# Kernel tuning notes

Hardware: AMD Instinct MI355X
Metric: run time of the kernel (lower is better)

The kernel has to match this reference:

```python
import jax, jax.numpy as jnp
import numpy as np

N_LEVELS = 16
N_FEATS = 2
LOG2_HASHMAP_SIZE = 19
BASE_RES = np.float32(16.0)
FINEST_RES = np.float32(512.0)
N_POINTS = 1048576

# corner offsets in (i, j, k) order: index = i*4 + j*2 + k, matching BOX_OFFSETS
OFFSETS = jnp.array([[i, j, k] for i in (0, 1) for j in (0, 1) for k in (0, 1)], dtype=jnp.int32)  # [8,3]
# spatial-hash primes from HashNeRF / Instant-NGP
PRIMES = np.array([1, 2654435761, 805459861], dtype=np.uint32)
HASH_MASK = np.uint32((1 << LOG2_HASHMAP_SIZE) - 1)


def _hash(coords):
    # coords: [..., 3] int32 grid coords -> [...] int32 table index
    c = coords.astype(jnp.uint32)
    h = (c[..., 0] * PRIMES[0]) ^ (c[..., 1] * PRIMES[1]) ^ (c[..., 2] * PRIMES[2])
    return (h & HASH_MASK).astype(jnp.int32)


def setup_inputs() -> dict:
    key = jax.random.key(0)
    k1, k2, k3 = jax.random.split(key, 3)
    x = jax.random.uniform(k1, (N_POINTS, 3), dtype=jnp.float32)  # points in unit box
    # nn.init.uniform_(weight, -1e-4, 1e-4), stacked over levels
    embeddings = jax.random.uniform(
        k2, (N_LEVELS, 1 << LOG2_HASHMAP_SIZE, N_FEATS),
        dtype=jnp.float32, minval=-1e-4, maxval=1e-4)
    level_weights = jnp.zeros((N_LEVELS,), dtype=jnp.float32)
    box_min = jnp.zeros((3,), dtype=jnp.float32)
    box_max = jnp.ones((3,), dtype=jnp.float32)
    return {"x": x, "embeddings": embeddings, "level_weights": level_weights,
            "box_min": box_min, "box_max": box_max}


def reference(x, embeddings, level_weights, box_min, box_max):
    n_levels = embeddings.shape[0]
    # per-level growth factor b = exp((log(finest) - log(base)) / (L-1)), static
    b = np.float32(np.exp((np.log(FINEST_RES) - np.log(BASE_RES)) / (n_levels - 1)))
    xc = jnp.clip(x, box_min, box_max)  # [N,3]
    outs = []
    for i in range(n_levels):
        res = np.float32(np.floor(BASE_RES * b ** i))  # static scalar resolution
        grid = (box_max - box_min) / res               # [3]
        bl = jnp.floor((xc - box_min) / grid).astype(jnp.int32)  # [N,3] bottom-left cell
        vmin = bl.astype(jnp.float32) * grid + box_min           # [N,3]
        vmax = vmin + grid                                       # [N,3]
        idx = _hash(bl[:, None, :] + OFFSETS[None, :, :])        # [N,8]
        emb = embeddings[i][idx]                                 # [N,8,F] gather
        # trilinear interpolation (weights use raw x, as in the torch module)
        w = (x - vmin) / (vmax - vmin)                           # [N,3]
        wx = w[:, 0][:, None, None]                              # [N,1,1]
        wy = w[:, 1][:, None]
        wz = w[:, 2][:, None]
        cx = emb[:, 0:4] * (1 - wx) + emb[:, 4:8] * wx           # [N,4,F] blend x
        c0 = cx[:, 0] * (1 - wy) + cx[:, 2] * wy                 # [N,F] blend y (k=0)
        c1 = cx[:, 1] * (1 - wy) + cx[:, 3] * wy                 # [N,F] blend y (k=1)
        c = c0 * (1 - wz) + c1 * wz                              # [N,F] blend z
        gate = jax.nn.sigmoid(level_weights[i])
        outs.append(c * gate)
    return jnp.concatenate(outs, axis=-1)  # [N, L*F]
```

## Files before the change

### kernel.cpp

```cpp
#include <hip/hip_runtime.h>
#include <stdint.h>


static constexpr int NP = 1048576;
static constexpr int NL = 16;
static constexpr int TPB = 256;
static constexpr uint32_t HMASK = (1u << 19) - 1u;

__constant__ float c_res[NL] = {16.f, 20.f, 25.f, 32.f, 40.f, 50.f, 64.f, 80.f,
                                101.f, 128.f, 161.f, 203.f, 256.f, 322.f, 406.f, 512.f};

__device__ __forceinline__ float2 enc_one(
    float x0, float x1, float x2,
    float b0, float b1, float b2,
    float B0, float B1, float B2,
    const float2* __restrict__ tab, float res, float gate)
{
    float g0 = (B0 - b0) / res;
    float g1 = (B1 - b1) / res;
    float g2 = (B2 - b2) / res;
    float xc0 = fminf(fmaxf(x0, b0), B0);
    float xc1 = fminf(fmaxf(x1, b1), B1);
    float xc2 = fminf(fmaxf(x2, b2), B2);
    float f0 = floorf((xc0 - b0) / g0);
    float f1 = floorf((xc1 - b1) / g1);
    float f2 = floorf((xc2 - b2) / g2);
    float v0 = f0 * g0 + b0;
    float v1 = f1 * g1 + b1;
    float v2 = f2 * g2 + b2;
    float w0 = (x0 - v0) / ((v0 + g0) - v0);
    float w1 = (x1 - v1) / ((v1 + g1) - v1);
    float w2 = (x2 - v2) / ((v2 + g2) - v2);

    uint32_t u0 = (uint32_t)(int)f0;
    uint32_t u1 = (uint32_t)(int)f1;
    uint32_t u2 = (uint32_t)(int)f2;
    uint32_t ya = u1 * 2654435761u, yb = (u1 + 1u) * 2654435761u;
    uint32_t za = u2 * 805459861u,  zb = (u2 + 1u) * 805459861u;
    uint32_t xa = u0, xb = u0 + 1u;

    float2 e000 = tab[(xa ^ ya ^ za) & HMASK];
    float2 e001 = tab[(xa ^ ya ^ zb) & HMASK];
    float2 e010 = tab[(xa ^ yb ^ za) & HMASK];
    float2 e011 = tab[(xa ^ yb ^ zb) & HMASK];
    float2 e100 = tab[(xb ^ ya ^ za) & HMASK];
    float2 e101 = tab[(xb ^ ya ^ zb) & HMASK];
    float2 e110 = tab[(xb ^ yb ^ za) & HMASK];
    float2 e111 = tab[(xb ^ yb ^ zb) & HMASK];

    float s0 = 1.f - w0, s1 = 1.f - w1, s2 = 1.f - w2;
    float cx00x = e000.x * s0 + e100.x * w0, cx00y = e000.y * s0 + e100.y * w0;
    float cx01x = e001.x * s0 + e101.x * w0, cx01y = e001.y * s0 + e101.y * w0;
    float cx10x = e010.x * s0 + e110.x * w0, cx10y = e010.y * s0 + e110.y * w0;
    float cx11x = e011.x * s0 + e111.x * w0, cx11y = e011.y * s0 + e111.y * w0;
    float c0x = cx00x * s1 + cx10x * w1, c0y = cx00y * s1 + cx10y * w1;
    float c1x = cx01x * s1 + cx11x * w1, c1y = cx01y * s1 + cx11y * w1;
    float ox = c0x * s2 + c1x * w2;
    float oy = c0y * s2 + c1y * w2;
    return make_float2(ox * gate, oy * gate);
}

__global__ __launch_bounds__(TPB) void k_enc(
    const float* __restrict__ x, const float* __restrict__ emb,
    const float* __restrict__ lw, const float* __restrict__ bmin,
    const float* __restrict__ bmax, float2* __restrict__ ws)
{
    int p = blockIdx.x * TPB + threadIdx.x;
    int l = blockIdx.y;
    float x0 = x[3 * p + 0], x1 = x[3 * p + 1], x2 = x[3 * p + 2];
    float b0 = bmin[0], b1 = bmin[1], b2 = bmin[2];
    float B0 = bmax[0], B1 = bmax[1], B2 = bmax[2];
    float res = c_res[l];
    float gate = 1.0f / (1.0f + expf(-lw[l]));
    const float2* tab = (const float2*)(emb + ((size_t)l << 20));
    float2 r = enc_one(x0, x1, x2, b0, b1, b2, B0, B1, B2, tab, res, gate);
    ws[(size_t)l * NP + p] = r;
}

__global__ __launch_bounds__(TPB) void k_tr(
    const float2* __restrict__ ws, float4* __restrict__ out)
{
    __shared__ float2 s[256][17];
    int t = threadIdx.x;
    size_t p0 = (size_t)blockIdx.x * 256;
#pragma unroll
    for (int l = 0; l < NL; ++l)
        s[t][l] = ws[(size_t)l * NP + p0 + (size_t)t];
    __syncthreads();
#pragma unroll
    for (int k = 0; k < 8; ++k) {
        int n = k * 256 + t;
        int q = n >> 3;
        int j = n & 7;
        float2 a = s[q][2 * j];
        float2 b = s[q][2 * j + 1];
        out[p0 * 8 + (size_t)n] = make_float4(a.x, a.y, b.x, b.y);
    }
}

__global__ __launch_bounds__(TPB) void k_fused(
    const float* __restrict__ x, const float* __restrict__ emb,
    const float* __restrict__ lw, const float* __restrict__ bmin,
    const float* __restrict__ bmax, float* __restrict__ out)
{
    int p = blockIdx.x * TPB + threadIdx.x;
    int g = blockIdx.y;
    float x0 = x[3 * p + 0], x1 = x[3 * p + 1], x2 = x[3 * p + 2];
    float b0 = bmin[0], b1 = bmin[1], b2 = bmin[2];
    float B0 = bmax[0], B1 = bmax[1], B2 = bmax[2];
    float2 o[4];
#pragma unroll
    for (int m = 0; m < 4; ++m) {
        int l = g * 4 + m;
        float res = c_res[l];
        float gate = 1.0f / (1.0f + expf(-lw[l]));
        const float2* tab = (const float2*)(emb + ((size_t)l << 20));
        o[m] = enc_one(x0, x1, x2, b0, b1, b2, B0, B1, B2, tab, res, gate);
    }
    float4* op = (float4*)(out + (size_t)p * 32 + g * 8);
    op[0] = make_float4(o[0].x, o[0].y, o[1].x, o[1].y);
    op[1] = make_float4(o[2].x, o[2].y, o[3].x, o[3].y);
}

extern "C" void kernel_launch(void* const* d_in, const int* in_sizes, int n_in,
                              void* d_out, int out_size, void* d_ws, size_t ws_size,
                              hipStream_t stream) {
    const float* x    = (const float*)d_in[0];
    const float* emb  = (const float*)d_in[1];
    const float* lw   = (const float*)d_in[2];
    const float* bmin = (const float*)d_in[3];
    const float* bmax = (const float*)d_in[4];
    float* out = (float*)d_out;

    const size_t ws_need = (size_t)NL * NP * 2 * sizeof(float);
    if (ws_size >= ws_need) {
        dim3 grid1(NP / TPB, NL);
        k_enc<<<grid1, TPB, 0, stream>>>(x, emb, lw, bmin, bmax, (float2*)d_ws);
        k_tr<<<NP / 256, TPB, 0, stream>>>((const float2*)d_ws, (float4*)out);
    } else {
        dim3 grid(NP / TPB, 4);
        k_fused<<<grid, TPB, 0, stream>>>(x, emb, lw, bmin, bmax, out);
    }
}
```

Measured before the change: 554.7 us.

## Fuse per-level encode and transpose into one all-levels kernel

Replaces the two-kernel scheme (per-level encode into a workspace, then a transpose kernel) with one kernel where each thread computes all 16 levels in two halves. It stages results through shared memory so output rows are written as coalesced float4. This removes the workspace write and read-back and one launch. In exchange, each block now gathers from all 16 hash tables, which loses per-level cache locality, and the grid has far fewer blocks with heavier threads.

```diff
diff --git a/kernel.cpp b/kernel.cpp
--- a/kernel.cpp
+++ b/kernel.cpp
@@ -60,66 +60,44 @@
     return make_float2(ox * gate, oy * gate);
 }
 
-__global__ __launch_bounds__(TPB) void k_enc(
+__global__ __launch_bounds__(TPB) void k_all(
     const float* __restrict__ x, const float* __restrict__ emb,
     const float* __restrict__ lw, const float* __restrict__ bmin,
-    const float* __restrict__ bmax, float2* __restrict__ ws)
+    const float* __restrict__ bmax, float4* __restrict__ out)
 {
-    int p = blockIdx.x * TPB + threadIdx.x;
-    int l = blockIdx.y;
+    __shared__ float2 s[256][9];
+    int t = threadIdx.x;
+    size_t p0 = (size_t)blockIdx.x * TPB;
+    size_t p = p0 + (size_t)t;
+
     float x0 = x[3 * p + 0], x1 = x[3 * p + 1], x2 = x[3 * p + 2];
     float b0 = bmin[0], b1 = bmin[1], b2 = bmin[2];
     float B0 = bmax[0], B1 = bmax[1], B2 = bmax[2];
-    float res = c_res[l];
-    float gate = 1.0f / (1.0f + expf(-lw[l]));
-    const float2* tab = (const float2*)(emb + ((size_t)l << 20));
-    float2 r = enc_one(x0, x1, x2, b0, b1, b2, B0, B1, B2, tab, res, gate);
-    ws[(size_t)l * NP + p] = r;
-}
 
-__global__ __launch_bounds__(TPB) void k_tr(
-    const float2* __restrict__ ws, float4* __restrict__ out)
-{
-    __shared__ float2 s[256][17];
-    int t = threadIdx.x;
-    size_t p0 = (size_t)blockIdx.x * 256;
 #pragma unroll
-    for (int l = 0; l < NL; ++l)
-        s[t][l] = ws[(size_t)l * NP + p0 + (size_t)t];
-    __syncthreads();
+    for (int h = 0; h < 2; ++h) {
+        float2 o[8];
 #pragma unroll
-    for (int k = 0; k < 8; ++k) {
-        int n = k * 256 + t;
-        int q = n >> 3;
-        int j = n & 7;
-        float2 a = s[q][2 * j];
-        float2 b = s[q][2 * j + 1];
-        out[p0 * 8 + (size_t)n] = make_float4(a.x, a.y, b.x, b.y);
+        for (int m = 0; m < 8; ++m) {
+            int l = h * 8 + m;
+            float gate = 1.0f / (1.0f + expf(-lw[l]));
+            const float2* tab = (const float2*)(emb + ((size_t)l << 20));
+            o[m] = enc_one(x0, x1, x2, b0, b1, b2, B0, B1, B2, tab, c_res[l], gate);
+        }
+        if (h) __syncthreads();
+#pragma unroll
+        for (int m = 0; m < 8; ++m) s[t][m] = o[m];
+        __syncthreads();
+#pragma unroll
+        for (int k = 0; k < 4; ++k) {
+            int mm = k * 256 + t;
+            int q = mm >> 2;
+            int j = mm & 3;
+            float2 a = s[q][2 * j];
+            float2 b = s[q][2 * j + 1];
+            out[(p0 + (size_t)q) * 8 + h * 4 + j] = make_float4(a.x, a.y, b.x, b.y);
+        }
     }
-}
-
-__global__ __launch_bounds__(TPB) void k_fused(
-    const float* __restrict__ x, const float* __restrict__ emb,
-    const float* __restrict__ lw, const float* __restrict__ bmin,
-    const float* __restrict__ bmax, float* __restrict__ out)
-{
-    int p = blockIdx.x * TPB + threadIdx.x;
-    int g = blockIdx.y;
-    float x0 = x[3 * p + 0], x1 = x[3 * p + 1], x2 = x[3 * p + 2];
-    float b0 = bmin[0], b1 = bmin[1], b2 = bmin[2];
-    float B0 = bmax[0], B1 = bmax[1], B2 = bmax[2];
-    float2 o[4];
-#pragma unroll
-    for (int m = 0; m < 4; ++m) {
-        int l = g * 4 + m;
-        float res = c_res[l];
-        float gate = 1.0f / (1.0f + expf(-lw[l]));
-        const float2* tab = (const float2*)(emb + ((size_t)l << 20));
-        o[m] = enc_one(x0, x1, x2, b0, b1, b2, B0, B1, B2, tab, res, gate);
-    }
-    float4* op = (float4*)(out + (size_t)p * 32 + g * 8);
-    op[0] = make_float4(o[0].x, o[0].y, o[1].x, o[1].y);
-    op[1] = make_float4(o[2].x, o[2].y, o[3].x, o[3].y);
 }
 
 extern "C" void kernel_launch(void* const* d_in, const int* in_sizes, int n_in,
@@ -130,15 +108,8 @@
     const float* lw   = (const float*)d_in[2];
     const float* bmin = (const float*)d_in[3];
     const float* bmax = (const float*)d_in[4];
-    float* out = (float*)d_out;
+    float4* out = (float4*)d_out;
+    (void)d_ws; (void)ws_size;
 
-    const size_t ws_need = (size_t)NL * NP * 2 * sizeof(float);
-    if (ws_size >= ws_need) {
-        dim3 grid1(NP / TPB, NL);
-        k_enc<<<grid1, TPB, 0, stream>>>(x, emb, lw, bmin, bmax, (float2*)d_ws);
-        k_tr<<<NP / 256, TPB, 0, stream>>>((const float2*)d_ws, (float4*)out);
-    } else {
-        dim3 grid(NP / TPB, 4);
-        k_fused<<<grid, TPB, 0, stream>>>(x, emb, lw, bmin, bmax, out);
-    }
+    k_all<<<NP / TPB, TPB, 0, stream>>>(x, emb, lw, bmin, bmax, out);
 }
```

After: 902.1 us. 62.6% more time.
